# Performance work log

Hardware: AMD Instinct MI355X
Metric: run time of the kernel (lower is better)

## Reference

```python
import jax, jax.numpy as jnp
import numpy as np

NEG = -1.0e9
OBS_VOCAB = 64
Y_CLASSES = 32


def setup_inputs() -> dict:
    key = jax.random.key(0)
    ks = jax.random.split(key, 6)
    B, V, N, O, Y, HID = 256, 32, 8192, OBS_VOCAB, Y_CLASSES, 128
    tables = jax.random.randint(ks[0], (B, V, N), 0, O)
    sigma = jax.random.randint(ks[1], (B, N), 0, Y)
    x = jax.random.randint(ks[2], (B,), 0, N)
    base_obs = jax.random.randint(ks[3], (B,), 0, O)
    W1 = jax.random.normal(ks[4], (3, HID), dtype=jnp.float32) * 0.1
    b1 = jnp.zeros((HID,), dtype=jnp.float32)
    W2 = jax.random.normal(ks[5], (HID, 1), dtype=jnp.float32) * 0.1
    b2 = jnp.zeros((1,), dtype=jnp.float32)
    return {"tables": tables, "sigma": sigma, "x": x, "base_obs": base_obs,
            "W1": W1, "b1": b1, "W2": W2, "b2": b2, "max_steps": 8}


def reference(tables, sigma, x, base_obs, W1, b1, W2, b2, max_steps):
    B, V, N = tables.shape
    bidx = jnp.arange(B)
    vidx = jnp.arange(V)

    def step(carry, _):
        m, stopped, used = carry  # m: [B,N] candidate mask, used: [B,V]
        mf = m.astype(jnp.float32)
        total = jnp.maximum(mf.sum(-1), 1.0)  # [B]
        # oracle features: expected posterior set size after asking each view
        # counts[b,v,o] = #candidates in m whose tables[b,v,:] label is o
        counts = jnp.zeros((B, V, OBS_VOCAB), jnp.float32).at[
            bidx[:, None, None], vidx[None, :, None], tables].add(mf[:, None, :])
        gathered = jnp.take_along_axis(counts, tables, axis=-1)  # [B,V,N]
        exp_size = (gathered * mf[:, None, :]).sum(-1) / total[:, None]  # [B,V]
        steps_f = jnp.log2(jnp.maximum(exp_size, 1.0))
        amb_f = exp_size - 1.0
        feat_views = jnp.stack([steps_f, amb_f, exp_size], axis=-1)  # [B,V,3]
        feat_views = feat_views.at[:, 0, 0].set(1000.0)  # oracle cfg forbid_view0
        closed = total <= 1.0
        stop_steps = jnp.where(closed, 0.0, 1000.0)  # allow_stop_only_if_closed
        feat_stop = jnp.stack([stop_steps, total - 1.0, total], axis=-1)[:, None, :]
        feat = jnp.clip(jnp.concatenate([feat_views, feat_stop], axis=1), -1000.0, 1000.0)
        h = jax.nn.gelu(feat @ W1 + b1, approximate=False)
        z_logits = jax.lax.stop_gradient((h @ W2 + b2)[..., 0])  # [B,V+1] (detached)
        # straight-through z on detached logits reduces to a hard one-hot constant
        z = jax.nn.one_hot(jnp.argmax(z_logits, axis=-1), V + 1, dtype=jnp.float32)
        logits = z.at[:, 0].set(NEG)  # forbid view 0
        used_full = jnp.concatenate([used, jnp.zeros((B, 1), bool)], axis=1)
        logits = jnp.where(used_full, NEG, logits)  # mask already-used views
        a = jnp.argmax(logits, axis=-1)
        a = jnp.where(stopped, V, a)
        is_stop = a == V
        ac = jnp.clip(a, 0, V - 1)
        r = tables[bidx, ac, x]
        r = jnp.where(is_stop, 0, r)
        m_new = m & (is_stop[:, None] | (tables[bidx, ac, :] == r[:, None]))
        used_new = used.at[bidx, ac].set(True)
        return (m_new, stopped | is_stop, used_new), (a, r)

    m0 = tables[:, 0, :] == base_obs[:, None]
    carry0 = (m0, jnp.zeros((B,), bool), jnp.zeros((B, V), bool))
    (m, _, _), (a_seq, r_seq) = jax.lax.scan(step, carry0, None, length=int(max_steps))
    actions = a_seq.T  # [B, T]
    responses = r_seq.T
    # predict_y: exact constructive posterior over classes from candidate mask
    w = m.astype(jnp.float32)
    denom = jnp.maximum(w.sum(-1, keepdims=True), 1.0)
    state_dist = w / denom  # [B,N]
    p_sig = jnp.zeros((B, Y_CLASSES), jnp.float32).at[bidx[:, None], sigma].add(state_dist)
    y_logits = jnp.log(jnp.maximum(p_sig, 1e-9))
    return actions, responses, y_logits
```

## Files before the change

kernel.cpp:

```cpp
#include <hip/hip_runtime.h>
#include <math.h>

#define HP 65

__device__ __forceinline__ float clip1000(float v) {
  return fminf(fmaxf(v, -1000.0f), 1000.0f);
}

__device__ __noinline__ float mlp16(const float* sw, float f0, float f1, float f2, int l) {
  const float* w1a = sw;        const float* w1b = sw + 128;
  const float* w1c = sw + 256;  const float* b1v = sw + 384;
  const float* w2v = sw + 512;
  float zp = 0.0f;
  {
    #pragma clang fp contract(off)
    #pragma clang loop unroll(disable)
    for (int k = l * 8; k < l * 8 + 8; ++k) {
      float pre = f0 * w1a[k] + f1 * w1b[k] + f2 * w1c[k] + b1v[k];
      float e = erff(pre / (float)M_SQRT2);
      float hg = 0.5f * pre * (1.0f + e);
      zp = zp + hg * w2v[k];
    }
  }
  zp += __shfl_xor(zp, 1);
  zp += __shfl_xor(zp, 2);
  zp += __shfl_xor(zp, 4);
  zp += __shfl_xor(zp, 8);
  return zp;
}

__launch_bounds__(1024, 1)
__global__ void sim_kernel(const int* __restrict__ tables,
                           const int* __restrict__ sigma,
                           const int* __restrict__ x,
                           const int* __restrict__ base_obs,
                           const float* __restrict__ W1,
                           const float* __restrict__ b1,
                           const float* __restrict__ W2,
                           const float* __restrict__ b2,
                           const int* __restrict__ max_steps_p,
                           float* __restrict__ out,
                           int B, int V, int N)
{
  const int b = blockIdx.x;
  const int tid = threadIdx.x;
  const int T = max_steps_p[0];

  __shared__ unsigned short s_pos[2][8192];
  __shared__ int s_gidx[8192];
  __shared__ int s_lab[256 * 33];
  __shared__ int s_h[32 * HP];
  __shared__ int s_surv[256];
  __shared__ float s_w[641];
  __shared__ float s_z[33];
  __shared__ float s_zc[6];
  __shared__ int s_used[32], s_ycnt[32], s_resp[32];
  __shared__ int s_nact, s_cnt, s_a, s_r;

  const int* tb = tables + (size_t)b * V * N;
  const int* sg = sigma + (size_t)b * N;
  const int bo = base_obs[b];
  const int xb = x[b];

  {
    float wv = 0.0f;
    if (tid < 384) wv = W1[tid];
    else if (tid < 512) wv = b1[tid - 384];
    else if (tid < 640) wv = W2[tid - 512];
    else if (tid == 640) wv = b2[0];
    if (tid <= 640) s_w[tid] = wv;
  }
  if (tid >= 704 && tid < 736) s_resp[tid - 704] = tb[(size_t)(tid - 704) * N + xb];
  if (tid < 32) { s_used[tid] = 0; s_ycnt[tid] = 0; }
  if (tid == 0) s_nact = 0;
  __syncthreads();

  if (tid < 928) {
    const int4* tb4 = (const int4*)tb;
    #pragma clang loop unroll(disable)
    for (int q = tid; q < (N >> 2); q += 928) {
      int4 v4 = tb4[q]; int base = q << 2;
      if (v4.x == bo) { int p = atomicAdd(&s_nact, 1); s_gidx[p] = base; }
      if (v4.y == bo) { int p = atomicAdd(&s_nact, 1); s_gidx[p] = base + 1; }
      if (v4.z == bo) { int p = atomicAdd(&s_nact, 1); s_gidx[p] = base + 2; }
      if (v4.w == bo) { int p = atomicAdd(&s_nact, 1); s_gidx[p] = base + 3; }
    }
  } else {
    const int g = (tid - 928) >> 4, l = (tid - 928) & 15;
    const float zcf[6][3] = {
      {1.0f, 1.0f, 2.0f},
      {0.0f, 0.0f, 1.0f},
      {1000.0f, 0.0f, 1.0f},
      {1000.0f, 1.0f, 2.0f},
      {0.0f, -1.0f, 0.0f},
      {1000.0f, -1.0f, 0.0f}};
    if (g < 6) {
      float zp = mlp16(s_w, zcf[g][0], zcf[g][1], zcf[g][2], l);
      if (l == 0) s_zc[g] = zp + s_w[640];
    }
  }
  __syncthreads();

  const int nact0 = s_nact;
  const bool cached = (nact0 <= 256);
  const int v32 = tid >> 5, g32 = tid & 31;
  #pragma clang loop unroll(disable)
  for (int j = tid; j < nact0; j += 1024) s_pos[0][j] = (unsigned short)j;

  auto labelOf = [&](int pos, int vv) -> int {
    return cached ? s_lab[pos * 33 + vv] : tb[(size_t)vv * N + s_gidx[pos]];
  };

  int cur = 0, t = 0, a = -1, r = 0;
  bool first = true, stopped = false, tail = false;

  while (true) {
    const bool need_hist = (t < T);
    const int nact = s_nact;

    if (need_hist) {
      #pragma clang loop unroll(disable)
      for (int i = tid; i < 32 * HP; i += 1024) s_h[i] = 0;
    }
    if (tid == 0) s_cnt = 0;
    __syncthreads();
    for (int c0 = 0; c0 < nact; c0 += 256) {
      const int cend = (nact < c0 + 256) ? nact : c0 + 256;
      if (first || v32 == a) {
        #pragma clang loop unroll(disable)
        for (int j = c0 + g32; j < cend; j += 32) {
          int pos = s_pos[cur][j];
          int lab;
          if (first) {
            lab = tb[(size_t)v32 * N + s_gidx[pos]];
            if (cached) s_lab[pos * 33 + v32] = lab;
          } else {
            lab = labelOf(pos, v32);
          }
          if (a >= 0 && v32 == a) {
            int sv = (lab == r);
            s_surv[j - c0] = sv;
            if (sv) { int p = atomicAdd(&s_cnt, 1); s_pos[cur ^ 1][p] = (unsigned short)pos; }
          }
        }
      }
      __syncthreads();
      if (cend >= nact && tid == 0 && a >= 0) s_nact = s_cnt;
      if (need_hist) {
        #pragma clang loop unroll(disable)
        for (int j = c0 + g32; j < cend; j += 32) {
          if (a < 0 || s_surv[j - c0]) {
            int pos = s_pos[cur][j];
            atomicAdd(&s_h[v32 * HP + labelOf(pos, v32)], 1);
          }
        }
      }
      __syncthreads();
    }
    if (a >= 0) cur ^= 1;
    first = false;

    if (s_nact <= 2) { tail = true; break; }
    if (t >= T) break;

    if (tid < 528) {
      const int view = tid >> 4, l = tid & 15;
      const float total = (float)s_nact;
      float f0, f1, f2;
      if (view == 32) {
        f0 = 1000.0f;
        f1 = clip1000(total - 1.0f);
        f2 = clip1000(total);
      } else {
        long long sumsq = 0;
        #pragma clang loop unroll(disable)
        for (int o = l * 4; o < l * 4 + 4; ++o) {
          long long c = (long long)s_h[view * HP + o];
          sumsq += c * c;
        }
        sumsq += __shfl_xor(sumsq, 1);
        sumsq += __shfl_xor(sumsq, 2);
        sumsq += __shfl_xor(sumsq, 4);
        sumsq += __shfl_xor(sumsq, 8);
        float es = (float)sumsq / total;
        float steps = (view == 0) ? 1000.0f : log2f(fmaxf(es, 1.0f));
        f0 = clip1000(steps); f1 = clip1000(es - 1.0f); f2 = clip1000(es);
      }
      float zp = mlp16(s_w, f0, f1, f2, l);
      if (l == 0) s_z[view] = zp + s_w[640];
    }
    __syncthreads();

    if (tid == 0) {
      int jstar = 0; float best = s_z[0];
      #pragma clang loop unroll(disable)
      for (int i = 1; i < 33; ++i) { float zz = s_z[i]; if (zz > best) { best = zz; jstar = i; } }
      int aa;
      if (jstar == 32 || (jstar >= 1 && !s_used[jstar])) aa = jstar;
      else {
        aa = 32;
        #pragma clang loop unroll(disable)
        for (int i = 1; i < 32; ++i)
          if (!s_used[i]) { aa = i; break; }
      }
      int rr = 0;
      if (aa != 32) { s_used[aa] = 1; rr = s_resp[aa]; }
      s_a = aa; s_r = rr;
      out[b * T + t] = (float)aa;
      out[(size_t)B * T + b * T + t] = (float)rr;
    }
    __syncthreads();
    a = s_a; r = s_r;
    ++t;
    if (a == 32) { stopped = true; break; }
  }

  if (stopped && tid == 0) {
    #pragma clang loop unroll(disable)
    for (int tt = t; tt < T; ++tt) {
      out[b * T + tt] = (float)V;
      out[(size_t)B * T + b * T + tt] = 0.0f;
    }
  }

  if (tail) {
    if (tid < 64) {
      const int lane = tid;
      int nact = s_nact;
      int p0 = (nact >= 1) ? (int)s_pos[cur][0] : 0;
      int p1 = (nact == 2) ? (int)s_pos[cur][1] : 0;
      unsigned usedmask;
      { bool ub = (lane < 32) && (s_used[lane] != 0);
        usedmask = (unsigned)__ballot(ub); }
      const float zA = s_zc[0], zB = s_zc[1], zC = s_zc[2],
                  zD = s_zc[3], zE = s_zc[4], zF = s_zc[5];
      unsigned esmask = 0;
      if (nact == 2) {
        int l0 = (lane < 32) ? labelOf(p0, lane) : 0;
        int l1 = (lane < 32) ? labelOf(p1, lane) : 0;
        esmask = (unsigned)__ballot(lane < 32 && (l0 == l1));
      }

      #pragma clang loop unroll(disable)
      for (; t < T; ++t) {
        int jstar; float best;
        if (nact == 2) {
          best = (esmask & 1u) ? zD : zC; jstar = 0;
          #pragma clang loop unroll(disable)
          for (int i = 1; i < 32; ++i) {
            float zz = ((esmask >> i) & 1u) ? zA : zB;
            if (zz > best) { best = zz; jstar = i; }
          }
          if (zD > best) { best = zD; jstar = 32; }
        } else if (nact == 1) {
          best = zC; jstar = 0;
          if (zB > best) { best = zB; jstar = 1; }
        } else {
          best = zF; jstar = 0;
          if (zE > best) { best = zE; jstar = 1; }
          if (zB > best) { best = zB; jstar = 32; }
        }
        int a2;
        if (jstar == 32 || (jstar >= 1 && !((usedmask >> jstar) & 1u))) a2 = jstar;
        else {
          unsigned freeb = ~usedmask & 0x7ffffffeu;
          a2 = freeb ? (int)__builtin_ctz(freeb) : 32;
        }
        if (a2 == 32) {
          if (lane == 0) {
            #pragma clang loop unroll(disable)
            for (int tt = t; tt < T; ++tt) {
              out[b * T + tt] = (float)V;
              out[(size_t)B * T + b * T + tt] = 0.0f;
            }
          }
          break;
        }
        usedmask |= (1u << a2);
        int r2 = s_resp[a2];
        if (lane == 0) {
          out[b * T + t] = (float)a2;
          out[(size_t)B * T + b * T + t] = (float)r2;
        }
        if (nact == 2) {
          bool k0 = (labelOf(p0, a2) == r2);
          bool k1 = (labelOf(p1, a2) == r2);
          if (k0 && k1) {  }
          else if (k0) { nact = 1; }
          else if (k1) { nact = 1; p0 = p1; }
          else { nact = 0; }
        } else if (nact == 1) {
          if (labelOf(p0, a2) != r2) nact = 0;
        }
      }
      if (lane == 0) {
        s_nact = nact;
        if (nact >= 1) s_pos[cur][0] = (unsigned short)p0;
      }
    }
    __syncthreads();
  }

  const int nfin = s_nact;
  #pragma clang loop unroll(disable)
  for (int j = tid; j < nfin; j += 1024) {
    atomicAdd(&s_ycnt[sg[s_gidx[s_pos[cur][j]]]], 1);
  }
  __syncthreads();
  if (tid < 32) {
    float denom = (float)(nfin > 1 ? nfin : 1);
    float q = 1.0f / denom;
    int c = s_ycnt[tid];
    float p = 0.0f;
    #pragma clang loop unroll(disable)
    for (int k = 0; k < c; ++k) p = p + q;
    out[(size_t)2 * B * T + b * 32 + tid] = logf(fmaxf(p, 1e-9f));
  }
}

extern "C" void kernel_launch(void* const* d_in, const int* in_sizes, int n_in,
                              void* d_out, int out_size, void* d_ws, size_t ws_size,
                              hipStream_t stream) {
  const int* tables   = (const int*)d_in[0];
  const int* sigma    = (const int*)d_in[1];
  const int* x        = (const int*)d_in[2];
  const int* base_obs = (const int*)d_in[3];
  const float* W1 = (const float*)d_in[4];
  const float* b1 = (const float*)d_in[5];
  const float* W2 = (const float*)d_in[6];
  const float* b2 = (const float*)d_in[7];
  const int* msteps = (const int*)d_in[8];
  float* out = (float*)d_out;

  const int B = in_sizes[2];
  const int N = in_sizes[1] / B;
  const int V = in_sizes[0] / (B * N);

  sim_kernel<<<dim3(B), dim3(1024), 0, stream>>>(
      tables, sigma, x, base_obs, W1, b1, W2, b2, msteps, out, B, V, N);
}
```

Measured before the change: 42.12 us.

## Restructure filter/histogram loop with in-place compaction and wave-parallel argmax

The per-step candidate filtering and histogram rebuild are reorganized. The initial label gather now fuses label caching with the first histogram build. Survivors are compacted in place into a single position buffer, which removes the double buffer and the s_surv staging. Each later histogram is spread over all 1024 threads instead of per-view warps. The serial argmax over 33 logits on thread 0 (in the main loop and the tail) becomes a wave-wide shuffle max plus ballot, and histogram zeroing overlaps with the action selection. Small inner loops are also unrolled. The in-place compaction relies on all of a chunk's reads finishing before its writes within one warp, which adds a correctness subtlety.

```diff
diff --git a/kernel.cpp b/kernel.cpp
--- a/kernel.cpp
+++ b/kernel.cpp
@@ -14,7 +14,7 @@
   float zp = 0.0f;
   {
     #pragma clang fp contract(off)
-    #pragma clang loop unroll(disable)
+    #pragma unroll
     for (int k = l * 8; k < l * 8 + 8; ++k) {
       float pre = f0 * w1a[k] + f1 * w1b[k] + f2 * w1c[k] + b1v[k];
       float e = erff(pre / (float)M_SQRT2);
@@ -27,6 +27,17 @@
   zp += __shfl_xor(zp, 4);
   zp += __shfl_xor(zp, 8);
   return zp;
+}
+
+__device__ __forceinline__ int firstmax64(float z) {
+  float m = z;
+  m = fmaxf(m, __shfl_xor(m, 1));
+  m = fmaxf(m, __shfl_xor(m, 2));
+  m = fmaxf(m, __shfl_xor(m, 4));
+  m = fmaxf(m, __shfl_xor(m, 8));
+  m = fmaxf(m, __shfl_xor(m, 16));
+  m = fmaxf(m, __shfl_xor(m, 32));
+  return (int)__builtin_ctzll(__ballot(z == m));
 }
 
 __launch_bounds__(1024, 1)
@@ -46,11 +57,10 @@
   const int tid = threadIdx.x;
   const int T = max_steps_p[0];
 
-  __shared__ unsigned short s_pos[2][8192];
+  __shared__ unsigned short s_pos[8192];
   __shared__ int s_gidx[8192];
   __shared__ int s_lab[256 * 33];
   __shared__ int s_h[32 * HP];
-  __shared__ int s_surv[256];
   __shared__ float s_w[641];
   __shared__ float s_z[33];
   __shared__ float s_zc[6];
@@ -71,6 +81,8 @@
     if (tid <= 640) s_w[tid] = wv;
   }
   if (tid >= 704 && tid < 736) s_resp[tid - 704] = tb[(size_t)(tid - 704) * N + xb];
+  #pragma clang loop unroll(disable)
+  for (int i = tid; i < 32 * HP; i += 1024) s_h[i] = 0;
   if (tid < 32) { s_used[tid] = 0; s_ycnt[tid] = 0; }
   if (tid == 0) s_nact = 0;
   __syncthreads();
@@ -104,68 +116,47 @@
   const int nact0 = s_nact;
   const bool cached = (nact0 <= 256);
   const int v32 = tid >> 5, g32 = tid & 31;
-  #pragma clang loop unroll(disable)
-  for (int j = tid; j < nact0; j += 1024) s_pos[0][j] = (unsigned short)j;
 
   auto labelOf = [&](int pos, int vv) -> int {
     return cached ? s_lab[pos * 33 + vv] : tb[(size_t)vv * N + s_gidx[pos]];
   };
 
-  int cur = 0, t = 0, a = -1, r = 0;
-  bool first = true, stopped = false, tail = false;
-
-  while (true) {
-    const bool need_hist = (t < T);
+  {
+    const int* row = tb + (size_t)v32 * N;
+    if (cached) {
+      int labs[8];
+      #pragma unroll
+      for (int u = 0; u < 8; ++u) {
+        int j = g32 + (u << 5);
+        if (j < nact0) labs[u] = row[s_gidx[j]];
+      }
+      #pragma unroll
+      for (int u = 0; u < 8; ++u) {
+        int j = g32 + (u << 5);
+        if (j < nact0) {
+          s_lab[j * 33 + v32] = labs[u];
+          atomicAdd(&s_h[v32 * HP + labs[u]], 1);
+        }
+      }
+    } else {
+      #pragma clang loop unroll(disable)
+      for (int j = g32; j < nact0; j += 32)
+        atomicAdd(&s_h[v32 * HP + row[s_gidx[j]]], 1);
+    }
+    #pragma clang loop unroll(disable)
+    for (int j = tid; j < nact0; j += 1024) s_pos[j] = (unsigned short)j;
+  }
+  __syncthreads();
+
+  int t = 0, a = -1, r = 0;
+  bool stopped = false, tail = false;
+  while (t < T) {
     const int nact = s_nact;
-
-    if (need_hist) {
-      #pragma clang loop unroll(disable)
-      for (int i = tid; i < 32 * HP; i += 1024) s_h[i] = 0;
-    }
-    if (tid == 0) s_cnt = 0;
-    __syncthreads();
-    for (int c0 = 0; c0 < nact; c0 += 256) {
-      const int cend = (nact < c0 + 256) ? nact : c0 + 256;
-      if (first || v32 == a) {
-        #pragma clang loop unroll(disable)
-        for (int j = c0 + g32; j < cend; j += 32) {
-          int pos = s_pos[cur][j];
-          int lab;
-          if (first) {
-            lab = tb[(size_t)v32 * N + s_gidx[pos]];
-            if (cached) s_lab[pos * 33 + v32] = lab;
-          } else {
-            lab = labelOf(pos, v32);
-          }
-          if (a >= 0 && v32 == a) {
-            int sv = (lab == r);
-            s_surv[j - c0] = sv;
-            if (sv) { int p = atomicAdd(&s_cnt, 1); s_pos[cur ^ 1][p] = (unsigned short)pos; }
-          }
-        }
-      }
-      __syncthreads();
-      if (cend >= nact && tid == 0 && a >= 0) s_nact = s_cnt;
-      if (need_hist) {
-        #pragma clang loop unroll(disable)
-        for (int j = c0 + g32; j < cend; j += 32) {
-          if (a < 0 || s_surv[j - c0]) {
-            int pos = s_pos[cur][j];
-            atomicAdd(&s_h[v32 * HP + labelOf(pos, v32)], 1);
-          }
-        }
-      }
-      __syncthreads();
-    }
-    if (a >= 0) cur ^= 1;
-    first = false;
-
-    if (s_nact <= 2) { tail = true; break; }
-    if (t >= T) break;
+    if (nact <= 2) { tail = true; break; }
 
     if (tid < 528) {
       const int view = tid >> 4, l = tid & 15;
-      const float total = (float)s_nact;
+      const float total = (float)nact;
       float f0, f1, f2;
       if (view == 32) {
         f0 = 1000.0f;
@@ -173,7 +164,7 @@
         f2 = clip1000(total);
       } else {
         long long sumsq = 0;
-        #pragma clang loop unroll(disable)
+        #pragma unroll
         for (int o = l * 4; o < l * 4 + 4; ++o) {
           long long c = (long long)s_h[view * HP + o];
           sumsq += c * c;
@@ -191,28 +182,62 @@
     }
     __syncthreads();
 
-    if (tid == 0) {
-      int jstar = 0; float best = s_z[0];
+    if (tid < 64) {
+      float z = (tid < 33) ? s_z[tid] : -3.0e9f;
+      int jstar = firstmax64(z);
+      unsigned usedm;
+      { bool ub = (tid < 32) && (s_used[tid] != 0);
+        usedm = (unsigned)__ballot(ub); }
+      int aa;
+      if (jstar == 32 || (jstar >= 1 && !((usedm >> jstar) & 1u))) aa = jstar;
+      else {
+        unsigned freeb = ~usedm & 0x7ffffffeu;
+        aa = freeb ? (int)__builtin_ctz(freeb) : 32;
+      }
+      if (tid == 0) {
+        int rr = 0;
+        if (aa != 32) { s_used[aa] = 1; rr = s_resp[aa]; }
+        s_a = aa; s_r = rr; s_cnt = 0;
+        out[b * T + t] = (float)aa;
+        out[(size_t)B * T + b * T + t] = (float)rr;
+      }
+    } else {
       #pragma clang loop unroll(disable)
-      for (int i = 1; i < 33; ++i) { float zz = s_z[i]; if (zz > best) { best = zz; jstar = i; } }
-      int aa;
-      if (jstar == 32 || (jstar >= 1 && !s_used[jstar])) aa = jstar;
-      else {
-        aa = 32;
-        #pragma clang loop unroll(disable)
-        for (int i = 1; i < 32; ++i)
-          if (!s_used[i]) { aa = i; break; }
-      }
-      int rr = 0;
-      if (aa != 32) { s_used[aa] = 1; rr = s_resp[aa]; }
-      s_a = aa; s_r = rr;
-      out[b * T + t] = (float)aa;
-      out[(size_t)B * T + b * T + t] = (float)rr;
+      for (int i = tid - 64; i < 32 * HP; i += 960) s_h[i] = 0;
     }
     __syncthreads();
+
     a = s_a; r = s_r;
     ++t;
     if (a == 32) { stopped = true; break; }
+
+    if (v32 == a) {
+      for (int c0 = 0; c0 < nact; c0 += 256) {
+        int poss[8], keep[8];
+        #pragma unroll
+        for (int u = 0; u < 8; ++u) {
+          int j = c0 + g32 + (u << 5);
+          poss[u] = (j < nact) ? (int)s_pos[j] : 0;
+          keep[u] = (j < nact) && (labelOf(poss[u], a) == r);
+        }
+        #pragma unroll
+        for (int u = 0; u < 8; ++u) {
+          if (keep[u]) { int p = atomicAdd(&s_cnt, 1); s_pos[p] = (unsigned short)poss[u]; }
+        }
+      }
+      if (g32 == 0) s_nact = s_cnt;
+    }
+    __syncthreads();
+
+    const int newn = s_nact;
+    if (t < T && newn > 2) {
+      #pragma clang loop unroll(disable)
+      for (int idx = tid; idx < newn * 32; idx += 1024) {
+        int j = idx >> 5, v = idx & 31;
+        atomicAdd(&s_h[v * HP + labelOf(s_pos[j], v)], 1);
+      }
+      __syncthreads();
+    }
   }
 
   if (stopped && tid == 0) {
@@ -227,8 +252,8 @@
     if (tid < 64) {
       const int lane = tid;
       int nact = s_nact;
-      int p0 = (nact >= 1) ? (int)s_pos[cur][0] : 0;
-      int p1 = (nact == 2) ? (int)s_pos[cur][1] : 0;
+      int p0 = (nact >= 1) ? (int)s_pos[0] : 0;
+      int p1 = (nact == 2) ? (int)s_pos[1] : 0;
       unsigned usedmask;
       { bool ub = (lane < 32) && (s_used[lane] != 0);
         usedmask = (unsigned)__ballot(ub); }
@@ -243,23 +268,21 @@
 
       #pragma clang loop unroll(disable)
       for (; t < T; ++t) {
-        int jstar; float best;
+        float zi;
         if (nact == 2) {
-          best = (esmask & 1u) ? zD : zC; jstar = 0;
-          #pragma clang loop unroll(disable)
-          for (int i = 1; i < 32; ++i) {
-            float zz = ((esmask >> i) & 1u) ? zA : zB;
-            if (zz > best) { best = zz; jstar = i; }
-          }
-          if (zD > best) { best = zD; jstar = 32; }
+          if (lane == 0)       zi = (esmask & 1u) ? zD : zC;
+          else if (lane < 32)  zi = ((esmask >> lane) & 1u) ? zA : zB;
+          else if (lane == 32) zi = zD;
+          else zi = -3.0e9f;
         } else if (nact == 1) {
-          best = zC; jstar = 0;
-          if (zB > best) { best = zB; jstar = 1; }
+          zi = (lane == 0) ? zC : (lane <= 32) ? zB : -3.0e9f;
         } else {
-          best = zF; jstar = 0;
-          if (zE > best) { best = zE; jstar = 1; }
-          if (zB > best) { best = zB; jstar = 32; }
-        }
+          if (lane == 0)       zi = zF;
+          else if (lane < 32)  zi = zE;
+          else if (lane == 32) zi = zB;
+          else zi = -3.0e9f;
+        }
+        int jstar = firstmax64(zi);
         int a2;
         if (jstar == 32 || (jstar >= 1 && !((usedmask >> jstar) & 1u))) a2 = jstar;
         else {
@@ -295,7 +318,7 @@
       }
       if (lane == 0) {
         s_nact = nact;
-        if (nact >= 1) s_pos[cur][0] = (unsigned short)p0;
+        if (nact >= 1) s_pos[0] = (unsigned short)p0;
       }
     }
     __syncthreads();
@@ -304,7 +327,7 @@
   const int nfin = s_nact;
   #pragma clang loop unroll(disable)
   for (int j = tid; j < nfin; j += 1024) {
-    atomicAdd(&s_ycnt[sg[s_gidx[s_pos[cur][j]]]], 1);
+    atomicAdd(&s_ycnt[sg[s_gidx[s_pos[j]]]], 1);
   }
   __syncthreads();
   if (tid < 32) {
```

New measurement: 37.21 us. -11.6%, faster.
